# Kernel optimization log

Hardware: AMD Instinct MI355X
Metric: run time of the kernel (lower is better)

The kernel has to match this reference:

```python
import jax, jax.numpy as jnp
import numpy as np

B = 128
VOCAB = 32000
EMB = 256
HID = 1024  # units*2 with units=512


def gru_step(x, h, Wi, Wr, bi, br):
    # Keras GRU, reset_after=True, gate order [z, r, h]
    gi = x @ Wi + bi          # [B, 3H]
    gr = h @ Wr + br          # [B, 3H]
    iz, ir, ih = jnp.split(gi, 3, axis=-1)
    rz, rr, rh = jnp.split(gr, 3, axis=-1)
    z = jax.nn.sigmoid(iz + rz)
    r = jax.nn.sigmoid(ir + rr)
    hh = jnp.tanh(ih + r * rh)
    return z * h + (1.0 - z) * hh


def setup_inputs() -> dict:
    key = jax.random.key(0)
    ks = jax.random.split(key, 16)
    s = 0.02
    inp = {
        "x": jax.random.randint(ks[0], (B, 1), 0, VOCAB),
        "h0": jax.random.normal(ks[1], (B, HID), jnp.float32),
        "h1": jax.random.normal(ks[2], (B, HID), jnp.float32),
        "emb": jax.random.normal(ks[3], (VOCAB, EMB), jnp.float32) * s,
        "Wi0": jax.random.normal(ks[4], (EMB, 3 * HID), jnp.float32) * s,
        "Wr0": jax.random.normal(ks[5], (HID, 3 * HID), jnp.float32) * s,
        "bi0": jnp.zeros((3 * HID,), jnp.float32),
        "br0": jnp.zeros((3 * HID,), jnp.float32),
        "Wi1": jax.random.normal(ks[6], (HID, 3 * HID), jnp.float32) * s,
        "Wr1": jax.random.normal(ks[7], (HID, 3 * HID), jnp.float32) * s,
        "bi1": jnp.zeros((3 * HID,), jnp.float32),
        "br1": jnp.zeros((3 * HID,), jnp.float32),
        "ffW": jax.random.normal(ks[8], (HID, VOCAB), jnp.float32) * s,
        "ffb": jnp.zeros((VOCAB,), jnp.float32),
    }
    return inp


def reference(x, h0, h1, emb, Wi0, Wr0, bi0, br0, Wi1, Wr1, bi1, br1, ffW, ffb):
    e = emb[x[:, 0]]                       # [B, EMB] (seq_len == 1)
    h0n = gru_step(e, h0, Wi0, Wr0, bi0, br0)   # [B, H]
    h1n = gru_step(h0n, h1, Wi1, Wr1, bi1, br1)  # [B, H]
    logits = h1n @ ffW + ffb               # [B, VOCAB]
    return logits, h0n, h1n
```

## Files before the change

### kernel.cpp

```cpp
#include <hip/hip_runtime.h>

#define HIDN 1024
#define G3 3072
#define NVOCAB 32000

typedef __bf16 bf16x8 __attribute__((ext_vector_type(8)));
typedef float f32x4 __attribute__((ext_vector_type(4)));
typedef unsigned short ushort4v __attribute__((ext_vector_type(4)));

__device__ __forceinline__ unsigned short f2bf(float f) {
  union { float f; unsigned int u; } v; v.f = f;
  unsigned int u = v.u;
  return (unsigned short)((u + 0x7fffu + ((u >> 16) & 1u)) >> 16);
}

__device__ __forceinline__ float sigmoidf_(float x) {
  return 1.0f / (1.0f + __expf(-x));
}

__device__ __forceinline__ void gload16(const void* g, void* l) {
  __builtin_amdgcn_global_load_lds(
      (const __attribute__((address_space(1))) unsigned int*)g,
      (__attribute__((address_space(3))) unsigned int*)l, 16, 0, 0);
}

__global__ __launch_bounds__(256) void prep_kernel(
    const float* __restrict__ h0, const float* __restrict__ h1,
    const float* __restrict__ emb, const int* __restrict__ x,
    ushort4v* __restrict__ h0b, ushort4v* __restrict__ h1b,
    ushort4v* __restrict__ eb) {
  int i = blockIdx.x * 256 + threadIdx.x;
  float4 v;
  ushort4v* dst;
  if (i < 32768) {
    v = ((const float4*)h0)[i];
    dst = h0b + i;
  } else if (i < 65536) {
    int j = i - 32768;
    v = ((const float4*)h1)[j];
    dst = h1b + j;
  } else {
    int j = i - 65536;
    int b = j >> 6, c = j & 63;
    v = ((const float4*)(emb + (size_t)x[b] * 256))[c];
    dst = eb + j;
  }
  ushort4v o;
  o[0] = f2bf(v.x); o[1] = f2bf(v.y); o[2] = f2bf(v.z); o[3] = f2bf(v.w);
  *dst = o;
}

__device__ __forceinline__ void gemm_rows32(
    const unsigned short* __restrict__ A, int lda, int k0, int Kh,
    const float* __restrict__ W, int ldw, int n0,
    const float* __restrict__ bias, float* __restrict__ C, int ldc,
    char* smem) {
  const int t = threadIdx.x;
  const int w = t >> 6, lane = t & 63;
  const int l15 = lane & 15, kg = lane >> 4;
  const int rh = w >> 1, ct = w & 1;

  f32x4 acc[4];
#pragma unroll
  for (int r = 0; r < 4; ++r) acc[r] = (f32x4)0.0f;

  const size_t srcB = (size_t)(w * 8 + (lane >> 3)) * ldw + n0 +
                      ((lane & 7) ^ ((w & 1) << 2)) * 4;
  size_t srcA[2];
#pragma unroll
  for (int m = 0; m < 2; ++m) {
    int g = (w * 2 + m) * 64 + lane;
    int row = g >> 2, uq = g & 3;
    int up = uq ^ ((row >> 1) & 3);
    srcA[m] = (size_t)row * lda + up * 8;
  }

  auto stage = [&](int c, int sel) {
    char* bb = smem + sel * 12288;
    char* ab = bb + 4096;
    int kbase = k0 + c * 32;
    gload16(W + (size_t)kbase * ldw + srcB, bb + w * 1024);
#pragma unroll
    for (int m = 0; m < 2; ++m)
      gload16(A + srcA[m] + kbase, ab + (w * 2 + m) * 1024);
  };

  const int NC = Kh >> 5;
  stage(0, 0);
  stage(1, 1);

  const int cl = ct * 16 + l15;
  for (int c = 0; c < NC; ++c) {
    if (c + 1 < NC)
      asm volatile("s_waitcnt vmcnt(3)" ::: "memory");
    else
      asm volatile("s_waitcnt vmcnt(0)" ::: "memory");
    __builtin_amdgcn_s_barrier();
    asm volatile("" ::: "memory");

    if (c + 2 < NC) stage(c + 2, (c + 2) % 3);

    int sel = c % 3;
    const float* bbf = (const float*)(smem + sel * 12288);
    const unsigned short* abf =
        (const unsigned short*)(smem + sel * 12288 + 4096);

    bf16x8 bfr;
#pragma unroll
    for (int j = 0; j < 8; ++j) {
      int r = kg * 8 + j;
      int q = (cl >> 2) ^ (((r >> 3) & 1) << 2);
      bfr[j] = (__bf16)bbf[r * 32 + q * 4 + (cl & 3)];
    }
#pragma unroll
    for (int rt = 0; rt < 4; ++rt) {
      int row = rh * 64 + rt * 16 + l15;
      bf16x8 af =
          *(const bf16x8*)(abf + row * 32 + ((kg ^ ((row >> 1) & 3)) << 3));
      acc[rt] =
          __builtin_amdgcn_mfma_f32_16x16x32_bf16(af, bfr, acc[rt], 0, 0, 0);
    }
  }

  const int col = n0 + cl;
  const float bs = bias ? bias[col] : 0.0f;
#pragma unroll
  for (int rt = 0; rt < 4; ++rt) {
    int rb = rh * 64 + rt * 16 + kg * 4;
#pragma unroll
    for (int j = 0; j < 4; ++j)
      C[(size_t)(rb + j) * ldc + col] = acc[rt][j] + bs;
  }
}

__global__ __launch_bounds__(256) void gru_gemms_kernel(
    const unsigned short* __restrict__ Xbf, int KX,
    const float* __restrict__ Wi, const float* __restrict__ bi,
    const unsigned short* __restrict__ Hbf,
    const float* __restrict__ Wr, const float* __restrict__ br,
    float* __restrict__ giP, float* __restrict__ grP) {
  __shared__ char smem[36864];
  int bid = blockIdx.x;
  int mat = bid / 192, rem = bid % 192;
  int ks = rem / 96, cb = rem % 96;
  if (mat == 0) {
    int Kh = KX >> 1;
    gemm_rows32(Xbf, KX, ks * Kh, Kh, Wi, G3, cb * 32, ks ? nullptr : bi,
                giP + (size_t)ks * 128 * G3, G3, smem);
  } else {
    gemm_rows32(Hbf, HIDN, ks * 512, 512, Wr, G3, cb * 32, ks ? nullptr : br,
                grP + (size_t)ks * 128 * G3, G3, smem);
  }
}

__global__ __launch_bounds__(256) void gates_kernel(
    const float* __restrict__ giP, const float* __restrict__ grP,
    const float* __restrict__ hfp, float* __restrict__ hout,
    ushort4v* __restrict__ hbf) {
  int i4 = blockIdx.x * 256 + threadIdx.x;
  int b = i4 >> 8, n = (i4 & 255) * 4;
  const float* g0 = giP + (size_t)b * G3;
  const float* g1 = g0 + (size_t)128 * G3;
  const float* r0 = grP + (size_t)b * G3;
  const float* r1 = r0 + (size_t)128 * G3;
  float4 izv = *(const float4*)(g0 + n);
  float4 izw = *(const float4*)(g1 + n);
  float4 rzv = *(const float4*)(r0 + n);
  float4 rzw = *(const float4*)(r1 + n);
  float4 irv = *(const float4*)(g0 + 1024 + n);
  float4 irw = *(const float4*)(g1 + 1024 + n);
  float4 rrv = *(const float4*)(r0 + 1024 + n);
  float4 rrw = *(const float4*)(r1 + 1024 + n);
  float4 ihv = *(const float4*)(g0 + 2048 + n);
  float4 ihw = *(const float4*)(g1 + 2048 + n);
  float4 rhv = *(const float4*)(r0 + 2048 + n);
  float4 rhw = *(const float4*)(r1 + 2048 + n);
  float4 hv = *(const float4*)(hfp + (size_t)b * HIDN + n);
  float4 ov;
  ushort4v obf;
#pragma unroll
  for (int j = 0; j < 4; ++j) {
    float iz = (&izv.x)[j] + (&izw.x)[j], rz = (&rzv.x)[j] + (&rzw.x)[j];
    float ir = (&irv.x)[j] + (&irw.x)[j], rr = (&rrv.x)[j] + (&rrw.x)[j];
    float ih = (&ihv.x)[j] + (&ihw.x)[j], rh = (&rhv.x)[j] + (&rhw.x)[j];
    float z = sigmoidf_(iz + rz);
    float r = sigmoidf_(ir + rr);
    float hh = tanhf(ih + r * rh);
    float h = (&hv.x)[j];
    float o = z * h + (1.0f - z) * hh;
    (&ov.x)[j] = o;
    obf[j] = f2bf(o);
  }
  *(float4*)(hout + (size_t)b * HIDN + n) = ov;
  hbf[i4] = obf;
}

__global__ __launch_bounds__(256) void ff_kernel(
    const unsigned short* __restrict__ A, const float* __restrict__ W,
    const float* __restrict__ bias, float* __restrict__ C) {
  __shared__ char smem[49152];
  const int n0 = blockIdx.x * 64;
  const int t = threadIdx.x;
  const int w = t >> 6, lane = t & 63;
  const int l15 = lane & 15, kg = lane >> 4;

  f32x4 acc[8];
#pragma unroll
  for (int r = 0; r < 8; ++r) acc[r] = (f32x4)0.0f;

  size_t srcB[2], srcA[2];
#pragma unroll
  for (int m = 0; m < 2; ++m) {
    int g = (w * 2 + m) * 64 + lane;
    {
      int r = g >> 4, q = g & 15;
      int p = q ^ (((r >> 3) & 1) << 2);
      srcB[m] = (size_t)r * NVOCAB + n0 + p * 4;
    }
    {
      int row = g >> 2, uq = g & 3;
      int up = uq ^ ((row >> 1) & 3);
      srcA[m] = (size_t)row * HIDN + up * 8;
    }
  }

  auto stage = [&](int c, int sel) {
    char* bb = smem + sel * 8192;
    char* ab = smem + 24576 + sel * 8192;
    int kbase = c * 32;
#pragma unroll
    for (int m = 0; m < 2; ++m)
      gload16(W + (size_t)kbase * NVOCAB + srcB[m], bb + (w * 2 + m) * 1024);
#pragma unroll
    for (int m = 0; m < 2; ++m)
      gload16(A + srcA[m] + kbase, ab + (w * 2 + m) * 1024);
  };

  stage(0, 0);
  stage(1, 1);

  const int NC = HIDN >> 5;
  const int cl = w * 16 + l15;
  for (int c = 0; c < NC; ++c) {
    if (c + 1 < NC)
      asm volatile("s_waitcnt vmcnt(4)" ::: "memory");
    else
      asm volatile("s_waitcnt vmcnt(0)" ::: "memory");
    __builtin_amdgcn_s_barrier();
    asm volatile("" ::: "memory");

    if (c + 2 < NC) stage(c + 2, (c + 2) % 3);

    int sel = c % 3;
    const float* bbf = (const float*)(smem + sel * 8192);
    const unsigned short* abf =
        (const unsigned short*)(smem + 24576 + sel * 8192);

    bf16x8 bfr;
#pragma unroll
    for (int j = 0; j < 8; ++j) {
      int r = kg * 8 + j;
      int q = (cl >> 2) ^ (((r >> 3) & 1) << 2);
      bfr[j] = (__bf16)bbf[r * 64 + q * 4 + (cl & 3)];
    }
#pragma unroll
    for (int rt = 0; rt < 8; ++rt) {
      int row = rt * 16 + l15;
      bf16x8 af =
          *(const bf16x8*)(abf + row * 32 + ((kg ^ ((row >> 1) & 3)) << 3));
      acc[rt] =
          __builtin_amdgcn_mfma_f32_16x16x32_bf16(af, bfr, acc[rt], 0, 0, 0);
    }
  }

  const int col = n0 + cl;
  const float bs = bias[col];
#pragma unroll
  for (int rt = 0; rt < 8; ++rt) {
    int rb = rt * 16 + kg * 4;
#pragma unroll
    for (int j = 0; j < 4; ++j)
      C[(size_t)(rb + j) * NVOCAB + col] = acc[rt][j] + bs;
  }
}

extern "C" void kernel_launch(void* const* d_in, const int* in_sizes, int n_in,
                              void* d_out, int out_size, void* d_ws,
                              size_t ws_size, hipStream_t stream) {
  const int* x = (const int*)d_in[0];
  const float* h0 = (const float*)d_in[1];
  const float* h1 = (const float*)d_in[2];
  const float* emb = (const float*)d_in[3];
  const float* Wi0 = (const float*)d_in[4];
  const float* Wr0 = (const float*)d_in[5];
  const float* bi0 = (const float*)d_in[6];
  const float* br0 = (const float*)d_in[7];
  const float* Wi1 = (const float*)d_in[8];
  const float* Wr1 = (const float*)d_in[9];
  const float* bi1 = (const float*)d_in[10];
  const float* br1 = (const float*)d_in[11];
  const float* ffW = (const float*)d_in[12];
  const float* ffb = (const float*)d_in[13];

  float* out = (float*)d_out;
  float* logits = out;
  float* h0n = out + 4096000;
  float* h1n = out + 4227072;

  unsigned short* h0b = (unsigned short*)d_ws;
  unsigned short* h1b = h0b + 131072;
  unsigned short* eb = h1b + 131072;
  unsigned short* h0nb = eb + 32768;
  unsigned short* h1nb = h0nb + 131072;
  float* giP = (float*)(h1nb + 131072);
  float* grP = giP + 2 * 128 * G3;

  prep_kernel<<<288, 256, 0, stream>>>(h0, h1, emb, x, (ushort4v*)h0b,
                                       (ushort4v*)h1b, (ushort4v*)eb);

  gru_gemms_kernel<<<384, 256, 0, stream>>>(eb, 256, Wi0, bi0, h0b, Wr0, br0,
                                            giP, grP);
  gates_kernel<<<128, 256, 0, stream>>>(giP, grP, h0, h0n, (ushort4v*)h0nb);

  gru_gemms_kernel<<<384, 256, 0, stream>>>(h0nb, 1024, Wi1, bi1, h1b, Wr1,
                                            br1, giP, grP);
  gates_kernel<<<128, 256, 0, stream>>>(giP, grP, h1, h1n, (ushort4v*)h1nb);

  ff_kernel<<<500, 256, 0, stream>>>(h1nb, ffW, ffb, logits);
}
```

Measured before the change: 56.35 us.

## Fuse prep and gate kernels into GRU GEMM kernels with last-block gating

Removes the separate fp32-to-bf16 prep kernel: the GEMM now loads fp32 A tiles (gathering embedding rows by token index for layer 0) into LDS and converts them to bf16 when building MFMA fragments. The gates computation is folded into the GEMM kernel, where the last of the 12 blocks touching each 32-column hidden group, found with an atomic counter, computes the gates. This cuts five launches to three plus a memset. The cost is doubled LDS traffic for fp32 A, more shared memory per block (60KB), and serialized gate work in the tail blocks.

Measured after the change: 155.7 us. 176% more time.

```diff
diff --git a/kernel.cpp b/kernel.cpp
--- a/kernel.cpp
+++ b/kernel.cpp
@@ -18,43 +18,25 @@
   return 1.0f / (1.0f + __expf(-x));
 }
 
+__device__ __forceinline__ float4 f4add(float4 a, float4 b) {
+  return make_float4(a.x + b.x, a.y + b.y, a.z + b.z, a.w + b.w);
+}
+
 __device__ __forceinline__ void gload16(const void* g, void* l) {
   __builtin_amdgcn_global_load_lds(
       (const __attribute__((address_space(1))) unsigned int*)g,
       (__attribute__((address_space(3))) unsigned int*)l, 16, 0, 0);
 }
 
-__global__ __launch_bounds__(256) void prep_kernel(
-    const float* __restrict__ h0, const float* __restrict__ h1,
-    const float* __restrict__ emb, const int* __restrict__ x,
-    ushort4v* __restrict__ h0b, ushort4v* __restrict__ h1b,
-    ushort4v* __restrict__ eb) {
-  int i = blockIdx.x * 256 + threadIdx.x;
-  float4 v;
-  ushort4v* dst;
-  if (i < 32768) {
-    v = ((const float4*)h0)[i];
-    dst = h0b + i;
-  } else if (i < 65536) {
-    int j = i - 32768;
-    v = ((const float4*)h1)[j];
-    dst = h1b + j;
-  } else {
-    int j = i - 65536;
-    int b = j >> 6, c = j & 63;
-    v = ((const float4*)(emb + (size_t)x[b] * 256))[c];
-    dst = eb + j;
-  }
-  ushort4v o;
-  o[0] = f2bf(v.x); o[1] = f2bf(v.y); o[2] = f2bf(v.z); o[3] = f2bf(v.w);
-  *dst = o;
-}
-
-__device__ __forceinline__ void gemm_rows32(
-    const unsigned short* __restrict__ A, int lda, int k0, int Kh,
-    const float* __restrict__ W, int ldw, int n0,
+template <bool AF32, bool GATHER>
+__device__ __forceinline__ void gemm32(
+    const void* __restrict__ Aptr, int lda, const int* __restrict__ rix,
+    int k0, int Kh, const float* __restrict__ W, int ldw, int n0,
     const float* __restrict__ bias, float* __restrict__ C, int ldc,
     char* smem) {
+  constexpr int ABYTES = AF32 ? 16384 : 8192;
+  constexpr int SBUF = 4096 + ABYTES;
+  constexpr int NA = AF32 ? 4 : 2;
   const int t = threadIdx.x;
   const int w = t >> 6, lane = t & 63;
   const int l15 = lane & 15, kg = lane >> 4;
@@ -66,23 +48,42 @@
 
   const size_t srcB = (size_t)(w * 8 + (lane >> 3)) * ldw + n0 +
                       ((lane & 7) ^ ((w & 1) << 2)) * 4;
-  size_t srcA[2];
-#pragma unroll
-  for (int m = 0; m < 2; ++m) {
-    int g = (w * 2 + m) * 64 + lane;
-    int row = g >> 2, uq = g & 3;
-    int up = uq ^ ((row >> 1) & 3);
-    srcA[m] = (size_t)row * lda + up * 8;
+  size_t srcA[NA];
+  if constexpr (AF32) {
+#pragma unroll
+    for (int m = 0; m < NA; ++m) {
+      int row = (w * 4 + m) * 8 + (lane >> 3);
+      size_t rb;
+      if constexpr (GATHER)
+        rb = (size_t)rix[row] * lda;
+      else
+        rb = (size_t)row * lda;
+      srcA[m] = rb + (((lane & 7) ^ (row & 7)) << 2);
+    }
+  } else {
+#pragma unroll
+    for (int m = 0; m < NA; ++m) {
+      int g = (w * 2 + m) * 64 + lane;
+      int row = g >> 2, uq = g & 3;
+      srcA[m] = (size_t)row * lda + ((uq ^ ((row >> 1) & 3)) << 3);
+    }
   }
 
   auto stage = [&](int c, int sel) {
-    char* bb = smem + sel * 12288;
+    char* bb = smem + sel * SBUF;
     char* ab = bb + 4096;
-    int kbase = k0 + c * 32;
+    const int kbase = k0 + c * 32;
     gload16(W + (size_t)kbase * ldw + srcB, bb + w * 1024);
-#pragma unroll
-    for (int m = 0; m < 2; ++m)
-      gload16(A + srcA[m] + kbase, ab + (w * 2 + m) * 1024);
+    if constexpr (AF32) {
+#pragma unroll
+      for (int m = 0; m < NA; ++m)
+        gload16((const float*)Aptr + srcA[m] + kbase, ab + (w * 4 + m) * 1024);
+    } else {
+#pragma unroll
+      for (int m = 0; m < NA; ++m)
+        gload16((const unsigned short*)Aptr + srcA[m] + kbase,
+                ab + (w * 2 + m) * 1024);
+    }
   };
 
   const int NC = Kh >> 5;
@@ -91,19 +92,22 @@
 
   const int cl = ct * 16 + l15;
   for (int c = 0; c < NC; ++c) {
-    if (c + 1 < NC)
-      asm volatile("s_waitcnt vmcnt(3)" ::: "memory");
-    else
+    if (c + 1 < NC) {
+      if constexpr (AF32)
+        asm volatile("s_waitcnt vmcnt(5)" ::: "memory");
+      else
+        asm volatile("s_waitcnt vmcnt(3)" ::: "memory");
+    } else {
       asm volatile("s_waitcnt vmcnt(0)" ::: "memory");
+    }
     __builtin_amdgcn_s_barrier();
     asm volatile("" ::: "memory");
 
     if (c + 2 < NC) stage(c + 2, (c + 2) % 3);
 
-    int sel = c % 3;
-    const float* bbf = (const float*)(smem + sel * 12288);
-    const unsigned short* abf =
-        (const unsigned short*)(smem + sel * 12288 + 4096);
+    const int sel = c % 3;
+    const float* bbf = (const float*)(smem + sel * SBUF);
+    const char* abf = smem + sel * SBUF + 4096;
 
     bf16x8 bfr;
 #pragma unroll
@@ -114,9 +118,20 @@
     }
 #pragma unroll
     for (int rt = 0; rt < 4; ++rt) {
-      int row = rh * 64 + rt * 16 + l15;
-      bf16x8 af =
-          *(const bf16x8*)(abf + row * 32 + ((kg ^ ((row >> 1) & 3)) << 3));
+      const int row = rh * 64 + rt * 16 + l15;
+      bf16x8 af;
+      if constexpr (AF32) {
+        const float* ar = (const float*)abf + row * 32;
+        float4 fa = *(const float4*)(ar + (((kg * 2 + 0) ^ (l15 & 7)) << 2));
+        float4 fb = *(const float4*)(ar + (((kg * 2 + 1) ^ (l15 & 7)) << 2));
+        af[0] = (__bf16)fa.x; af[1] = (__bf16)fa.y;
+        af[2] = (__bf16)fa.z; af[3] = (__bf16)fa.w;
+        af[4] = (__bf16)fb.x; af[5] = (__bf16)fb.y;
+        af[6] = (__bf16)fb.z; af[7] = (__bf16)fb.w;
+      } else {
+        af = *(const bf16x8*)((const unsigned short*)abf + row * 32 +
+                              ((kg ^ ((row >> 1) & 3)) << 3));
+      }
       acc[rt] =
           __builtin_amdgcn_mfma_f32_16x16x32_bf16(af, bfr, acc[rt], 0, 0, 0);
     }
@@ -126,73 +141,77 @@
   const float bs = bias ? bias[col] : 0.0f;
 #pragma unroll
   for (int rt = 0; rt < 4; ++rt) {
-    int rb = rh * 64 + rt * 16 + kg * 4;
+    const int rb = rh * 64 + rt * 16 + kg * 4;
 #pragma unroll
     for (int j = 0; j < 4; ++j)
       C[(size_t)(rb + j) * ldc + col] = acc[rt][j] + bs;
   }
 }
 
-__global__ __launch_bounds__(256) void gru_gemms_kernel(
-    const unsigned short* __restrict__ Xbf, int KX,
-    const float* __restrict__ Wi, const float* __restrict__ bi,
-    const unsigned short* __restrict__ Hbf,
-    const float* __restrict__ Wr, const float* __restrict__ br,
-    float* __restrict__ giP, float* __restrict__ grP) {
-  __shared__ char smem[36864];
-  int bid = blockIdx.x;
-  int mat = bid / 192, rem = bid % 192;
-  int ks = rem / 96, cb = rem % 96;
+template <bool XF32>
+__global__ __launch_bounds__(256) void gru_layer_kernel(
+    const void* __restrict__ X, int KX, const int* __restrict__ xidx,
+    const float* __restrict__ H, const float* __restrict__ Wi,
+    const float* __restrict__ bi, const float* __restrict__ Wr,
+    const float* __restrict__ br, float* __restrict__ giP,
+    float* __restrict__ grP, const float* __restrict__ hprev,
+    float* __restrict__ hout, ushort4v* __restrict__ hbf,
+    int* __restrict__ cnt) {
+  __shared__ char smem[3 * 20480];
+  __shared__ int isLast;
+  const int bid = blockIdx.x;
+  const int mat = bid / 192, rem = bid % 192;
+  const int ks = rem / 96, cb = rem % 96;
   if (mat == 0) {
-    int Kh = KX >> 1;
-    gemm_rows32(Xbf, KX, ks * Kh, Kh, Wi, G3, cb * 32, ks ? nullptr : bi,
-                giP + (size_t)ks * 128 * G3, G3, smem);
+    const int Kh = KX >> 1;
+    gemm32<XF32, XF32>(X, KX, xidx, ks * Kh, Kh, Wi, G3, cb * 32,
+                       ks ? nullptr : bi, giP + (size_t)ks * 128 * G3, G3,
+                       smem);
   } else {
-    gemm_rows32(Hbf, HIDN, ks * 512, 512, Wr, G3, cb * 32, ks ? nullptr : br,
-                grP + (size_t)ks * 128 * G3, G3, smem);
-  }
-}
-
-__global__ __launch_bounds__(256) void gates_kernel(
-    const float* __restrict__ giP, const float* __restrict__ grP,
-    const float* __restrict__ hfp, float* __restrict__ hout,
-    ushort4v* __restrict__ hbf) {
-  int i4 = blockIdx.x * 256 + threadIdx.x;
-  int b = i4 >> 8, n = (i4 & 255) * 4;
-  const float* g0 = giP + (size_t)b * G3;
-  const float* g1 = g0 + (size_t)128 * G3;
-  const float* r0 = grP + (size_t)b * G3;
-  const float* r1 = r0 + (size_t)128 * G3;
-  float4 izv = *(const float4*)(g0 + n);
-  float4 izw = *(const float4*)(g1 + n);
-  float4 rzv = *(const float4*)(r0 + n);
-  float4 rzw = *(const float4*)(r1 + n);
-  float4 irv = *(const float4*)(g0 + 1024 + n);
-  float4 irw = *(const float4*)(g1 + 1024 + n);
-  float4 rrv = *(const float4*)(r0 + 1024 + n);
-  float4 rrw = *(const float4*)(r1 + 1024 + n);
-  float4 ihv = *(const float4*)(g0 + 2048 + n);
-  float4 ihw = *(const float4*)(g1 + 2048 + n);
-  float4 rhv = *(const float4*)(r0 + 2048 + n);
-  float4 rhw = *(const float4*)(r1 + 2048 + n);
-  float4 hv = *(const float4*)(hfp + (size_t)b * HIDN + n);
-  float4 ov;
-  ushort4v obf;
-#pragma unroll
-  for (int j = 0; j < 4; ++j) {
-    float iz = (&izv.x)[j] + (&izw.x)[j], rz = (&rzv.x)[j] + (&rzw.x)[j];
-    float ir = (&irv.x)[j] + (&irw.x)[j], rr = (&rrv.x)[j] + (&rrw.x)[j];
-    float ih = (&ihv.x)[j] + (&ihw.x)[j], rh = (&rhv.x)[j] + (&rhw.x)[j];
-    float z = sigmoidf_(iz + rz);
-    float r = sigmoidf_(ir + rr);
-    float hh = tanhf(ih + r * rh);
-    float h = (&hv.x)[j];
-    float o = z * h + (1.0f - z) * hh;
-    (&ov.x)[j] = o;
-    obf[j] = f2bf(o);
-  }
-  *(float4*)(hout + (size_t)b * HIDN + n) = ov;
-  hbf[i4] = obf;
+    gemm32<true, false>(H, HIDN, nullptr, ks * 512, 512, Wr, G3, cb * 32,
+                        ks ? nullptr : br, grP + (size_t)ks * 128 * G3, G3,
+                        smem);
+  }
+
+  __threadfence();
+  __syncthreads();
+  const int hg = cb & 31;
+  if (threadIdx.x == 0) isLast = (atomicAdd(cnt + hg, 1) == 11);
+  __syncthreads();
+  if (!isLast) return;
+  __threadfence();
+
+  const int t = threadIdx.x;
+  const int lr = t >> 3;
+  const int col = hg * 32 + (t & 7) * 4;
+#pragma unroll
+  for (int p = 0; p < 4; ++p) {
+    const int row = p * 32 + lr;
+    const float* g0 = giP + (size_t)row * G3 + col;
+    const float* g1 = g0 + (size_t)128 * G3;
+    const float* r0 = grP + (size_t)row * G3 + col;
+    const float* r1 = r0 + (size_t)128 * G3;
+    float4 iz = f4add(*(const float4*)g0, *(const float4*)g1);
+    float4 ir = f4add(*(const float4*)(g0 + 1024), *(const float4*)(g1 + 1024));
+    float4 ih = f4add(*(const float4*)(g0 + 2048), *(const float4*)(g1 + 2048));
+    float4 rz = f4add(*(const float4*)r0, *(const float4*)r1);
+    float4 rr = f4add(*(const float4*)(r0 + 1024), *(const float4*)(r1 + 1024));
+    float4 rh = f4add(*(const float4*)(r0 + 2048), *(const float4*)(r1 + 2048));
+    float4 hv = *(const float4*)(hprev + (size_t)row * HIDN + col);
+    float4 ov;
+    ushort4v ob;
+#pragma unroll
+    for (int j = 0; j < 4; ++j) {
+      float z = sigmoidf_((&iz.x)[j] + (&rz.x)[j]);
+      float r = sigmoidf_((&ir.x)[j] + (&rr.x)[j]);
+      float hh = tanhf((&ih.x)[j] + r * (&rh.x)[j]);
+      float o = z * (&hv.x)[j] + (1.0f - z) * hh;
+      (&ov.x)[j] = o;
+      ob[j] = f2bf(o);
+    }
+    *(float4*)(hout + (size_t)row * HIDN + col) = ov;
+    hbf[((size_t)row * HIDN + col) >> 2] = ob;
+  }
 }
 
 __global__ __launch_bounds__(256) void ff_kernel(
@@ -307,24 +326,21 @@
   float* h0n = out + 4096000;
   float* h1n = out + 4227072;
 
-  unsigned short* h0b = (unsigned short*)d_ws;
-  unsigned short* h1b = h0b + 131072;
-  unsigned short* eb = h1b + 131072;
-  unsigned short* h0nb = eb + 32768;
+  float* giP = (float*)d_ws;
+  float* grP = giP + 2 * 128 * G3;
+  unsigned short* h0nb = (unsigned short*)(grP + 2 * 128 * G3);
   unsigned short* h1nb = h0nb + 131072;
-  float* giP = (float*)(h1nb + 131072);
-  float* grP = giP + 2 * 128 * G3;
-
-  prep_kernel<<<288, 256, 0, stream>>>(h0, h1, emb, x, (ushort4v*)h0b,
-                                       (ushort4v*)h1b, (ushort4v*)eb);
-
-  gru_gemms_kernel<<<384, 256, 0, stream>>>(eb, 256, Wi0, bi0, h0b, Wr0, br0,
-                                            giP, grP);
-  gates_kernel<<<128, 256, 0, stream>>>(giP, grP, h0, h0n, (ushort4v*)h0nb);
-
-  gru_gemms_kernel<<<384, 256, 0, stream>>>(h0nb, 1024, Wi1, bi1, h1b, Wr1,
-                                            br1, giP, grP);
-  gates_kernel<<<128, 256, 0, stream>>>(giP, grP, h1, h1n, (ushort4v*)h1nb);
+  int* cnt = (int*)(h1nb + 131072);
+
+  hipMemsetAsync(cnt, 0, 64 * sizeof(int), stream);
+
+  gru_layer_kernel<true><<<384, 256, 0, stream>>>(
+      emb, 256, x, h0, Wi0, bi0, Wr0, br0, giP, grP, h0, h0n,
+      (ushort4v*)h0nb, cnt);
+
+  gru_layer_kernel<false><<<384, 256, 0, stream>>>(
+      h0nb, 1024, nullptr, h1, Wi1, bi1, Wr1, br1, giP, grP, h1, h1n,
+      (ushort4v*)h1nb, cnt + 32);
 
   ff_kernel<<<500, 256, 0, stream>>>(h1nb, ffW, ffb, logits);
 }
```
